# Kernel tuning notes

Hardware: AMD Instinct MI355X
Metric: run time of the kernel (lower is better)

The kernel has to match this reference:

```python
import jax, jax.numpy as jnp
import numpy as np

N, DIN, DOUT = 8192, 512, 256


def setup_inputs() -> dict:
    key = jax.random.key(0)
    ks = jax.random.split(key, 8)
    s_in = 1.0 / np.sqrt(DIN)   # ~ torch Linear default init scale
    s_out = 1.0 / np.sqrt(DOUT)
    return {
        "x": jax.random.normal(ks[0], (N, DIN), jnp.float32),
        "Wm": jax.random.normal(ks[1], (DIN, DOUT), jnp.float32) * s_in,
        "Wn": jax.random.normal(ks[2], (DIN, DOUT), jnp.float32) * s_in,
        "Wr": jax.random.normal(ks[3], (DIN, DOUT), jnp.float32) * s_in,
        "Wt": jax.random.normal(ks[4], (DIN, DOUT), jnp.float32) * s_in,
        "Wrg": jax.random.normal(ks[5], (DOUT, DOUT), jnp.float32) * s_out,
        "brg": jnp.zeros((DOUT,), jnp.float32),
        "Wlg": jax.random.normal(ks[6], (DOUT, DOUT), jnp.float32) * s_out,
        "blg": jnp.zeros((DOUT,), jnp.float32),
        "Wp": jax.random.normal(ks[7], (DOUT, 1), jnp.float32) * s_out,
        "bp": jnp.zeros((1,), jnp.float32),
    }


def reference(x, Wm, Wn, Wr, Wt, Wrg, brg, Wlg, blg, Wp, bp):
    n = x.shape[0]
    xm = x @ Wm                      # [N, 256]
    xn = x @ Wn                      # [N, 256]
    # pairwise Euclidean distance via GEMM trick (avoids O(N^2*D) diff tensor)
    sq = (jnp.sum(xm * xm, axis=-1)[:, None]
          + jnp.sum(xn * xn, axis=-1)[None, :]
          - 2.0 * (xm @ xn.T))       # [N, N]
    dist = jnp.sqrt(jnp.maximum(sq, 0.0)) * 0.5
    exps = jnp.exp(-dist) / (n / 64.0)
    eye = jnp.eye(n, dtype=x.dtype)
    adj = exps * (1.0 - eye) + eye   # unit diagonal, scaled off-diagonal
    xr = adj @ (x @ Wr)              # graph conv: [N,N]@[N,256]
    xl = x @ Wt
    w = jax.nn.sigmoid(xr @ Wrg + brg + xl @ Wlg + blg)
    feat = (1.0 - w) * xr + w * xl   # gated fusion
    score = feat @ Wp + bp           # [N, 1]
    return adj, score
```

## Files before the change

### kernel.cpp

```cpp
#include <hip/hip_runtime.h>
#include <stdint.h>

typedef __attribute__((ext_vector_type(8))) short bf16x8;
typedef __attribute__((ext_vector_type(4))) float f32x4;

__device__ __forceinline__ unsigned short f2bf(float f){
  unsigned u = __float_as_uint(f);
  u += 0x7FFFu + ((u >> 16) & 1u);
  return (unsigned short)(u >> 16);
}
__device__ __forceinline__ float bf2f(unsigned short s){
  return __uint_as_float(((unsigned)s) << 16);
}

__device__ __forceinline__ int lds_off(int r, int b){
  return r * 128 + (b ^ ((r & 7) << 4));
}

__device__ __forceinline__ void cp16(const unsigned short* g, unsigned short* l){
  __builtin_amdgcn_global_load_lds(
      (const __attribute__((address_space(1))) unsigned int*)g,
      (__attribute__((address_space(3))) unsigned int*)l, 16, 0, 0);
}

template<int ROWS, int NT>
__device__ __forceinline__ void stage_async(unsigned short* lds, const unsigned short* g,
                                            long row0, long stride, long k0, int tid){
#pragma unroll
  for (int c = tid; c < ROWS * 8; c += NT){
    int r = c >> 3, s = c & 7;
    int ss = s ^ (r & 7);
    cp16(g + (row0 + r) * stride + k0 + ss * 8, lds + (long)(c & ~63) * 8);
  }
}

template<int ROWS, int NT>
__device__ __forceinline__ void stage_f32_nt(unsigned short* lds, const float* g,
                                             long row0, long stride, long k0, int tid){
#pragma unroll
  for (int c = tid; c < ROWS * 8; c += NT){
    int r = c >> 3, s = c & 7;
    const f32x4* src = (const f32x4*)(g + (row0 + r) * stride + k0 + s * 8);
    f32x4 v0 = __builtin_nontemporal_load(src);
    f32x4 v1 = __builtin_nontemporal_load(src + 1);
    unsigned short t[8] = { f2bf(v0[0]), f2bf(v0[1]), f2bf(v0[2]), f2bf(v0[3]),
                            f2bf(v1[0]), f2bf(v1[1]), f2bf(v1[2]), f2bf(v1[3]) };
    *(uint4*)((char*)lds + lds_off(r, s * 16)) = *(const uint4*)t;
  }
}

__device__ __forceinline__ int xcd_swz(int bid, int nwg){
  int q = nwg >> 3;
  return (bid & 7) * q + (bid >> 3);
}

__global__ __launch_bounds__(256) void k_prep(const float* x, const float* Wm, const float* Wn,
    const float* Wr, const float* Wt, const float* Wrg, const float* Wlg, const float* bp,
    unsigned short* WT, unsigned short* WcatT, unsigned short* xbf, float* score){
  long id = (long)blockIdx.x * 256 + threadIdx.x;
  if (id < 1024L * 512){
    int n = (int)(id >> 9), k = (int)(id & 511);
    const float* W = (n < 256) ? Wm : ((n < 512) ? Wn : ((n < 768) ? Wr : Wt));
    WT[id] = f2bf(W[(long)k * 256 + (n & 255)]);
  }
  if (id < 256L * 512){
    int n = (int)(id >> 9), k = (int)(id & 511);
    WcatT[id] = f2bf(k < 256 ? Wrg[(long)k * 256 + n] : Wlg[(long)(k - 256) * 256 + n]);
  }
  if (id < 8192) score[id] = bp[0];
  long xe = id * 8;
  float4 v0 = *(const float4*)(x + xe);
  float4 v1 = *(const float4*)(x + xe + 4);
  unsigned short t[8] = { f2bf(v0.x), f2bf(v0.y), f2bf(v0.z), f2bf(v0.w),
                          f2bf(v1.x), f2bf(v1.y), f2bf(v1.z), f2bf(v1.w) };
  *(uint4*)(xbf + xe) = *(const uint4*)t;
}

__global__ __launch_bounds__(256, 3) void k_gemmA(const unsigned short* xbf, const unsigned short* WT,
    unsigned short* xm, unsigned short* xn, unsigned short* xwrT, unsigned short* xl){
  __shared__ unsigned short ldsA[128 * 64];
  __shared__ unsigned short ldsB[128 * 64];
  int tid = threadIdx.x, lane = tid & 63, w = tid >> 6;
  int r = lane & 15, gq = lane >> 4;
  int wi = w >> 1, wc = w & 1;
  int swz = xcd_swz(blockIdx.x, 512);
  int bm = swz & 63, bn = swz >> 6;

  f32x4 acc[4][4];
  f32x4 zero = {0.f, 0.f, 0.f, 0.f};
#pragma unroll
  for (int m = 0; m < 4; ++m)
#pragma unroll
    for (int n = 0; n < 4; ++n) acc[m][n] = zero;

  for (int k0 = 0; k0 < 512; k0 += 64){
    __syncthreads();
    stage_async<128, 256>(ldsA, xbf, (long)bm * 128, 512, k0, tid);
    stage_async<128, 256>(ldsB, WT, (long)bn * 128, 512, k0, tid);
    __syncthreads();
#pragma unroll
    for (int ks = 0; ks < 2; ++ks){
      int bb = ks * 64 + gq * 16;
      bf16x8 a[4], b[4];
#pragma unroll
      for (int m = 0; m < 4; ++m)
        a[m] = *(const bf16x8*)((const char*)ldsA + lds_off(wi * 64 + m * 16 + r, bb));
#pragma unroll
      for (int n = 0; n < 4; ++n)
        b[n] = *(const bf16x8*)((const char*)ldsB + lds_off(wc * 64 + n * 16 + r, bb));
#pragma unroll
      for (int m = 0; m < 4; ++m)
#pragma unroll
        for (int n = 0; n < 4; ++n)
          acc[m][n] = __builtin_amdgcn_mfma_f32_16x16x32_bf16(b[n], a[m], acc[m][n], 0, 0, 0);
    }
  }
#pragma unroll
  for (int m = 0; m < 4; ++m){
    int i = bm * 128 + wi * 64 + m * 16 + r;
#pragma unroll
    for (int n = 0; n < 4; ++n){
      int ng = bn * 128 + wc * 64 + n * 16 + gq * 4;
      int sector = ng >> 8, nc = ng & 255;
      unsigned short p[4] = { f2bf(acc[m][n][0]), f2bf(acc[m][n][1]),
                              f2bf(acc[m][n][2]), f2bf(acc[m][n][3]) };
      if (sector == 2){
#pragma unroll
        for (int q = 0; q < 4; ++q) xwrT[(long)(nc + q) * 8192 + i] = p[q];
      } else {
        unsigned short* dst = sector == 0 ? xm : (sector == 1 ? xn : xl);
        *(uint2*)(dst + (long)i * 256 + nc) = *(const uint2*)p;
      }
    }
  }
}

__global__ __launch_bounds__(256) void k_norms(const unsigned short* xm, const unsigned short* xn,
                                               float* nm, float* nn){
  int w = threadIdx.x >> 6, lane = threadIdx.x & 63;
  int row = blockIdx.x * 4 + w;
  const unsigned short* src = (row < 8192) ? xm : xn;
  int rr = row & 8191;
  unsigned short v[4];
  *(uint2*)v = *(const uint2*)(src + (long)rr * 256 + lane * 4);
  float s = 0.f;
#pragma unroll
  for (int t = 0; t < 4; ++t){ float f = bf2f(v[t]); s += f * f; }
#pragma unroll
  for (int o = 32; o; o >>= 1) s += __shfl_xor(s, o);
  if (lane == 0) ((row < 8192) ? nm : nn)[rr] = s;
}

__global__ __launch_bounds__(256, 4) void k_adj(const unsigned short* xm, const unsigned short* xn,
    const float* nm, const float* nn, float* adj){
  __shared__ char smem[32768];
  unsigned short* ldsA = (unsigned short*)smem;
  unsigned short* ldsB = (unsigned short*)(smem + 16384);
  f32x4* ldsOut = (f32x4*)smem;

  int tid = threadIdx.x, lane = tid & 63, w = tid >> 6;
  int r = lane & 15, gq = lane >> 4;
  int wi = w >> 1, wj = w & 1;
  int swz = xcd_swz(blockIdx.x, 4096);
  int bm = swz & 63, bn = swz >> 6;

  f32x4 acc1[4][4];
  f32x4 zero = {0.f, 0.f, 0.f, 0.f};
#pragma unroll
  for (int m = 0; m < 4; ++m)
#pragma unroll
    for (int n = 0; n < 4; ++n) acc1[m][n] = zero;

  for (int k0 = 0; k0 < 256; k0 += 64){
    __syncthreads();
    stage_async<128, 256>(ldsA, xm, (long)bm * 128, 256, k0, tid);
    stage_async<128, 256>(ldsB, xn, (long)bn * 128, 256, k0, tid);
    __syncthreads();
#pragma unroll
    for (int ks = 0; ks < 2; ++ks){
      int bb = ks * 64 + gq * 16;
      bf16x8 a[4], b[4];
#pragma unroll
      for (int m = 0; m < 4; ++m)
        a[m] = *(const bf16x8*)((const char*)ldsA + lds_off(wi * 64 + m * 16 + r, bb));
#pragma unroll
      for (int n = 0; n < 4; ++n)
        b[n] = *(const bf16x8*)((const char*)ldsB + lds_off(wj * 64 + n * 16 + r, bb));
#pragma unroll
      for (int m = 0; m < 4; ++m)
#pragma unroll
        for (int n = 0; n < 4; ++n)
          acc1[m][n] = __builtin_amdgcn_mfma_f32_16x16x32_bf16(b[n], a[m], acc1[m][n], 0, 0, 0);
    }
  }

  float nmi[4];
#pragma unroll
  for (int m = 0; m < 4; ++m) nmi[m] = nm[bm * 128 + wi * 64 + m * 16 + r];
#pragma unroll
  for (int n = 0; n < 4; ++n){
    int jb = bn * 128 + wj * 64 + n * 16 + gq * 4;
    float4 nn4 = *(const float4*)(nn + jb);
    const float nnq[4] = { nn4.x, nn4.y, nn4.z, nn4.w };
#pragma unroll
    for (int m = 0; m < 4; ++m){
      int i = bm * 128 + wi * 64 + m * 16 + r;
#pragma unroll
      for (int q = 0; q < 4; ++q){
        float sq = nmi[m] + nnq[q] - 2.f * acc1[m][n][q];
        float d = sqrtf(fmaxf(sq, 0.f)) * 0.5f;
        acc1[m][n][q] = (i == jb + q) ? 1.f : __expf(-d) * (1.f / 128.f);
      }
    }
  }

#pragma unroll
  for (int p = 0; p < 2; ++p){
    __syncthreads();
    if (wi == p){
#pragma unroll
      for (int m = 0; m < 4; ++m){
        int row64 = m * 16 + r;
#pragma unroll
        for (int n = 0; n < 4; ++n){
          int slot = wj * 16 + n * 4 + gq;
          ldsOut[row64 * 32 + (slot ^ (row64 & 7))] = acc1[m][n];
        }
      }
    }
    __syncthreads();
#pragma unroll
    for (int c = 0; c < 8; ++c){
      int rr = w * 16 + ((lane >> 3) << 1) + (c & 1);
      int slot = (c >> 1) * 8 + (lane & 7);
      f32x4 v = ldsOut[rr * 32 + (slot ^ (rr & 7))];
      long grow = (long)(bm * 128 + p * 64 + rr) * 8192 + bn * 128 + slot * 4;
      __builtin_nontemporal_store(v, (f32x4*)(adj + grow));
    }
  }
}

__global__ __launch_bounds__(512, 2) void k_xr(const float* adj,
    const unsigned short* xwrT, float* partial, int klen, int nblk){
  __shared__ unsigned short ldsA[128 * 64];
  __shared__ unsigned short ldsB[256 * 64];
  int tid = threadIdx.x, lane = tid & 63, w = tid >> 6;
  int r = lane & 15, gq = lane >> 4;
  int wi = w >> 2, wc = w & 3;
  int swz = xcd_swz(blockIdx.x, nblk);
  int bm = swz & 63, sp = swz >> 6;
  long j0 = (long)sp * klen;

  f32x4 acc[4][4];
  f32x4 zero = {0.f, 0.f, 0.f, 0.f};
#pragma unroll
  for (int m = 0; m < 4; ++m)
#pragma unroll
    for (int n = 0; n < 4; ++n) acc[m][n] = zero;

  for (int k0 = 0; k0 < klen; k0 += 64){
    __syncthreads();
    stage_f32_nt<128, 512>(ldsA, adj, (long)bm * 128, 8192, j0 + k0, tid);
    stage_async<256, 512>(ldsB, xwrT, 0, 8192, j0 + k0, tid);
    __syncthreads();
#pragma unroll
    for (int ks = 0; ks < 2; ++ks){
      int bb = ks * 64 + gq * 16;
      bf16x8 a[4], b[4];
#pragma unroll
      for (int m = 0; m < 4; ++m)
        a[m] = *(const bf16x8*)((const char*)ldsA + lds_off(wi * 64 + m * 16 + r, bb));
#pragma unroll
      for (int n = 0; n < 4; ++n)
        b[n] = *(const bf16x8*)((const char*)ldsB + lds_off(wc * 64 + n * 16 + r, bb));
#pragma unroll
      for (int m = 0; m < 4; ++m)
#pragma unroll
        for (int n = 0; n < 4; ++n)
          acc[m][n] = __builtin_amdgcn_mfma_f32_16x16x32_bf16(b[n], a[m], acc[m][n], 0, 0, 0);
    }
  }
  float* dst = partial + (long)sp * 8192 * 256;
#pragma unroll
  for (int m = 0; m < 4; ++m){
    int i = bm * 128 + wi * 64 + m * 16 + r;
#pragma unroll
    for (int n = 0; n < 4; ++n){
      int cb = wc * 64 + n * 16 + gq * 4;
      __builtin_nontemporal_store(acc[m][n], (f32x4*)(dst + (long)i * 256 + cb));
    }
  }
}

__global__ __launch_bounds__(256) void k_reduce_xr(const float* partial, unsigned short* xr, int S){
  long idx = ((long)blockIdx.x * 256 + threadIdx.x) * 4;
  f32x4 a = __builtin_nontemporal_load((const f32x4*)(partial + idx));
  for (int s = 1; s < S; ++s){
    f32x4 b = __builtin_nontemporal_load((const f32x4*)(partial + (long)s * 8192 * 256 + idx));
    a += b;
  }
  unsigned short p[4] = { f2bf(a[0]), f2bf(a[1]), f2bf(a[2]), f2bf(a[3]) };
  *(uint2*)(xr + idx) = make_uint2((unsigned)p[0] | ((unsigned)p[1] << 16),
                                   (unsigned)p[2] | ((unsigned)p[3] << 16));
}

__global__ __launch_bounds__(512, 2) void k_gate(const unsigned short* xr, const unsigned short* xl,
    const unsigned short* WcatT, const float* brg, const float* blg,
    const float* Wp, float* score){
  __shared__ unsigned short ldsA[128 * 64];
  __shared__ unsigned short ldsB[256 * 64];
  int tid = threadIdx.x, lane = tid & 63, w = tid >> 6;
  int r = lane & 15, gq = lane >> 4;
  int wi = w >> 2, wc = w & 3;
  int bm = blockIdx.x;

  f32x4 acc[4][4];
  f32x4 zero = {0.f, 0.f, 0.f, 0.f};
#pragma unroll
  for (int m = 0; m < 4; ++m)
#pragma unroll
    for (int n = 0; n < 4; ++n) acc[m][n] = zero;

  for (int k0 = 0; k0 < 512; k0 += 64){
    const unsigned short* A = (k0 < 256) ? xr : xl;
    __syncthreads();
    stage_async<128, 512>(ldsA, A, (long)bm * 128, 256, k0 & 255, tid);
    stage_async<256, 512>(ldsB, WcatT, 0, 512, k0, tid);
    __syncthreads();
#pragma unroll
    for (int ks = 0; ks < 2; ++ks){
      int bb = ks * 64 + gq * 16;
      bf16x8 a[4], b[4];
#pragma unroll
      for (int m = 0; m < 4; ++m)
        a[m] = *(const bf16x8*)((const char*)ldsA + lds_off(wi * 64 + m * 16 + r, bb));
#pragma unroll
      for (int n = 0; n < 4; ++n)
        b[n] = *(const bf16x8*)((const char*)ldsB + lds_off(wc * 64 + n * 16 + r, bb));
#pragma unroll
      for (int m = 0; m < 4; ++m)
#pragma unroll
        for (int n = 0; n < 4; ++n)
          acc[m][n] = __builtin_amdgcn_mfma_f32_16x16x32_bf16(b[n], a[m], acc[m][n], 0, 0, 0);
    }
  }
#pragma unroll
  for (int m = 0; m < 4; ++m){
    int i = bm * 128 + wi * 64 + m * 16 + r;
    float part = 0.f;
#pragma unroll
    for (int n = 0; n < 4; ++n){
      int cb = wc * 64 + n * 16 + gq * 4;
      float4 b4  = *(const float4*)(brg + cb);
      float4 l4  = *(const float4*)(blg + cb);
      float4 wp4 = *(const float4*)(Wp + cb);
      unsigned short xr4[4], xl4[4];
      *(uint2*)xr4 = *(const uint2*)(xr + (long)i * 256 + cb);
      *(uint2*)xl4 = *(const uint2*)(xl + (long)i * 256 + cb);
      const float bq[4] = { b4.x, b4.y, b4.z, b4.w };
      const float lq[4] = { l4.x, l4.y, l4.z, l4.w };
      const float pq[4] = { wp4.x, wp4.y, wp4.z, wp4.w };
#pragma unroll
      for (int q = 0; q < 4; ++q){
        float arg = acc[m][n][q] + bq[q] + lq[q];
        float wv = 1.f / (1.f + __expf(-arg));
        float feat = (1.f - wv) * bf2f(xr4[q]) + wv * bf2f(xl4[q]);
        part += feat * pq[q];
      }
    }
    part += __shfl_xor(part, 16);
    part += __shfl_xor(part, 32);
    if (gq == 0) atomicAdd(score + i, part);
  }
}

extern "C" void kernel_launch(void* const* d_in, const int* in_sizes, int n_in,
                              void* d_out, int out_size, void* d_ws, size_t ws_size,
                              hipStream_t stream){
  const float* x   = (const float*)d_in[0];
  const float* Wm  = (const float*)d_in[1];
  const float* Wn  = (const float*)d_in[2];
  const float* Wr  = (const float*)d_in[3];
  const float* Wt  = (const float*)d_in[4];
  const float* Wrg = (const float*)d_in[5];
  const float* brg = (const float*)d_in[6];
  const float* Wlg = (const float*)d_in[7];
  const float* blg = (const float*)d_in[8];
  const float* Wp  = (const float*)d_in[9];
  const float* bp  = (const float*)d_in[10];

  float* adj   = (float*)d_out;
  float* score = adj + 8192L * 8192;

  char* wsb = (char*)d_ws;
  unsigned short* xm    = (unsigned short*)(wsb);
  unsigned short* xn    = (unsigned short*)(wsb + (4L  << 20));
  unsigned short* xwrT  = (unsigned short*)(wsb + (8L  << 20));
  unsigned short* xl    = (unsigned short*)(wsb + (12L << 20));
  unsigned short* xr    = (unsigned short*)(wsb + (16L << 20));
  float*          nm    = (float*)         (wsb + (20L << 20));
  float*          nn    = nm + 8192;
  unsigned short* WT    = (unsigned short*)(wsb + (21L << 20));
  unsigned short* WcatT = (unsigned short*)(wsb + (22L << 20));
  unsigned short* xbf   = (unsigned short*)(wsb + (23L << 20));
  float*          partial = (float*)(wsb + (31L << 20));

  int NS = 1;
  size_t base = 31L << 20;
  if      (ws_size >= base + 8 * (8L << 20)) NS = 8;
  else if (ws_size >= base + 4 * (8L << 20)) NS = 4;
  else if (ws_size >= base + 2 * (8L << 20)) NS = 2;

  k_prep  <<<2048, 256, 0, stream>>>(x, Wm, Wn, Wr, Wt, Wrg, Wlg, bp, WT, WcatT, xbf, score);
  k_gemmA <<<512, 256, 0, stream>>>(xbf, WT, xm, xn, xwrT, xl);
  k_norms <<<4096, 256, 0, stream>>>(xm, xn, nm, nn);
  k_adj   <<<4096, 256, 0, stream>>>(xm, xn, nm, nn, adj);
  k_xr    <<<64 * NS, 512, 0, stream>>>(adj, xwrT, partial, 8192 / NS, 64 * NS);
  k_reduce_xr<<<2048, 256, 0, stream>>>(partial, xr, NS);
  k_gate  <<<64, 512, 0, stream>>>(xr, xl, WcatT, brg, blg, Wp, score);
}
```

Measured before the change: 307.3 us.

## Fuse adjacency computation with graph-conv GEMM, keeping adj tile in LDS

Merges the adjacency kernel and the adj@xWr GEMM into one kernel. Each block loops over column tiles of its row band, computes the exp-distance tile, stores it to LDS as bf16 and writes it to global memory. It then uses that LDS tile directly as the A operand of the second GEMM, so the full fp32 adj matrix is no longer read back from HBM. The costs are fewer, longer-running blocks (64*NSP), serialized per-block work, and an adj output that is now rounded to bf16 before being widened to fp32. It also adds s_setprio around the MFMA loops.

```diff
diff --git a/kernel.cpp b/kernel.cpp
--- a/kernel.cpp
+++ b/kernel.cpp
@@ -16,6 +16,9 @@
 __device__ __forceinline__ int lds_off(int r, int b){
   return r * 128 + (b ^ ((r & 7) << 4));
 }
+__device__ __forceinline__ int ldsP_off(int r, int b){
+  return r * 256 + (b ^ ((r & 7) << 4));
+}
 
 __device__ __forceinline__ void cp16(const unsigned short* g, unsigned short* l){
   __builtin_amdgcn_global_load_lds(
@@ -31,21 +34,6 @@
     int r = c >> 3, s = c & 7;
     int ss = s ^ (r & 7);
     cp16(g + (row0 + r) * stride + k0 + ss * 8, lds + (long)(c & ~63) * 8);
-  }
-}
-
-template<int ROWS, int NT>
-__device__ __forceinline__ void stage_f32_nt(unsigned short* lds, const float* g,
-                                             long row0, long stride, long k0, int tid){
-#pragma unroll
-  for (int c = tid; c < ROWS * 8; c += NT){
-    int r = c >> 3, s = c & 7;
-    const f32x4* src = (const f32x4*)(g + (row0 + r) * stride + k0 + s * 8);
-    f32x4 v0 = __builtin_nontemporal_load(src);
-    f32x4 v1 = __builtin_nontemporal_load(src + 1);
-    unsigned short t[8] = { f2bf(v0[0]), f2bf(v0[1]), f2bf(v0[2]), f2bf(v0[3]),
-                            f2bf(v1[0]), f2bf(v1[1]), f2bf(v1[2]), f2bf(v1[3]) };
-    *(uint4*)((char*)lds + lds_off(r, s * 16)) = *(const uint4*)t;
   }
 }
 
@@ -151,143 +139,133 @@
   if (lane == 0) ((row < 8192) ? nm : nn)[rr] = s;
 }
 
-__global__ __launch_bounds__(256, 4) void k_adj(const unsigned short* xm, const unsigned short* xn,
-    const float* nm, const float* nn, float* adj){
-  __shared__ char smem[32768];
+__global__ __launch_bounds__(256, 2) void k_fused(
+    const unsigned short* xm, const unsigned short* xn,
+    const float* nm, const float* nn, const unsigned short* xwrT,
+    float* adj, float* partial, int ntiles, int nsp){
+  __shared__ char smem[65536];
   unsigned short* ldsA = (unsigned short*)smem;
   unsigned short* ldsB = (unsigned short*)(smem + 16384);
-  f32x4* ldsOut = (f32x4*)smem;
+  unsigned short* ldsW = (unsigned short*)smem;
+  char*           ldsP = smem + 32768;
 
   int tid = threadIdx.x, lane = tid & 63, w = tid >> 6;
   int r = lane & 15, gq = lane >> 4;
   int wi = w >> 1, wj = w & 1;
-  int swz = xcd_swz(blockIdx.x, 4096);
-  int bm = swz & 63, bn = swz >> 6;
-
-  f32x4 acc1[4][4];
+  int sp = blockIdx.x % nsp, bm = blockIdx.x / nsp;
+
   f32x4 zero = {0.f, 0.f, 0.f, 0.f};
+  f32x4 acc2[4][8];
 #pragma unroll
   for (int m = 0; m < 4; ++m)
 #pragma unroll
-    for (int n = 0; n < 4; ++n) acc1[m][n] = zero;
-
-  for (int k0 = 0; k0 < 256; k0 += 64){
-    __syncthreads();
-    stage_async<128, 256>(ldsA, xm, (long)bm * 128, 256, k0, tid);
-    stage_async<128, 256>(ldsB, xn, (long)bn * 128, 256, k0, tid);
-    __syncthreads();
-#pragma unroll
-    for (int ks = 0; ks < 2; ++ks){
-      int bb = ks * 64 + gq * 16;
-      bf16x8 a[4], b[4];
-#pragma unroll
-      for (int m = 0; m < 4; ++m)
-        a[m] = *(const bf16x8*)((const char*)ldsA + lds_off(wi * 64 + m * 16 + r, bb));
-#pragma unroll
-      for (int n = 0; n < 4; ++n)
-        b[n] = *(const bf16x8*)((const char*)ldsB + lds_off(wj * 64 + n * 16 + r, bb));
-#pragma unroll
-      for (int m = 0; m < 4; ++m)
+    for (int n = 0; n < 8; ++n) acc2[m][n] = zero;
+
+  float nmi[4];
+#pragma unroll
+  for (int m = 0; m < 4; ++m) nmi[m] = nm[bm * 128 + wi * 64 + m * 16 + r];
+
+  for (int t = 0; t < ntiles; ++t){
+    int bn = sp * ntiles + t;
+    f32x4 acc1[4][4];
+#pragma unroll
+    for (int m = 0; m < 4; ++m)
+#pragma unroll
+      for (int n = 0; n < 4; ++n) acc1[m][n] = zero;
+
+    for (int k0 = 0; k0 < 256; k0 += 64){
+      __syncthreads();
+      stage_async<128, 256>(ldsA, xm, (long)bm * 128, 256, k0, tid);
+      stage_async<128, 256>(ldsB, xn, (long)bn * 128, 256, k0, tid);
+      __syncthreads();
+      __builtin_amdgcn_s_setprio(1);
+#pragma unroll
+      for (int ks = 0; ks < 2; ++ks){
+        int bb = ks * 64 + gq * 16;
+        bf16x8 a[4], b[4];
+#pragma unroll
+        for (int m = 0; m < 4; ++m)
+          a[m] = *(const bf16x8*)((const char*)ldsA + lds_off(wi * 64 + m * 16 + r, bb));
 #pragma unroll
         for (int n = 0; n < 4; ++n)
-          acc1[m][n] = __builtin_amdgcn_mfma_f32_16x16x32_bf16(b[n], a[m], acc1[m][n], 0, 0, 0);
-    }
-  }
-
-  float nmi[4];
-#pragma unroll
-  for (int m = 0; m < 4; ++m) nmi[m] = nm[bm * 128 + wi * 64 + m * 16 + r];
-#pragma unroll
-  for (int n = 0; n < 4; ++n){
-    int jb = bn * 128 + wj * 64 + n * 16 + gq * 4;
-    float4 nn4 = *(const float4*)(nn + jb);
-    const float nnq[4] = { nn4.x, nn4.y, nn4.z, nn4.w };
-#pragma unroll
-    for (int m = 0; m < 4; ++m){
-      int i = bm * 128 + wi * 64 + m * 16 + r;
-#pragma unroll
-      for (int q = 0; q < 4; ++q){
-        float sq = nmi[m] + nnq[q] - 2.f * acc1[m][n][q];
-        float d = sqrtf(fmaxf(sq, 0.f)) * 0.5f;
-        acc1[m][n][q] = (i == jb + q) ? 1.f : __expf(-d) * (1.f / 128.f);
-      }
-    }
-  }
-
-#pragma unroll
-  for (int p = 0; p < 2; ++p){
-    __syncthreads();
-    if (wi == p){
+          b[n] = *(const bf16x8*)((const char*)ldsB + lds_off(wj * 64 + n * 16 + r, bb));
+#pragma unroll
+        for (int m = 0; m < 4; ++m)
+#pragma unroll
+          for (int n = 0; n < 4; ++n)
+            acc1[m][n] = __builtin_amdgcn_mfma_f32_16x16x32_bf16(b[n], a[m], acc1[m][n], 0, 0, 0);
+      }
+      __builtin_amdgcn_s_setprio(0);
+    }
+
+#pragma unroll
+    for (int n = 0; n < 4; ++n){
+      int jl0 = wj * 64 + n * 16 + gq * 4;
+      int jb = bn * 128 + jl0;
+      float4 nn4 = *(const float4*)(nn + jb);
+      const float nnq[4] = { nn4.x, nn4.y, nn4.z, nn4.w };
 #pragma unroll
       for (int m = 0; m < 4; ++m){
-        int row64 = m * 16 + r;
-#pragma unroll
-        for (int n = 0; n < 4; ++n){
-          int slot = wj * 16 + n * 4 + gq;
-          ldsOut[row64 * 32 + (slot ^ (row64 & 7))] = acc1[m][n];
+        int il = wi * 64 + m * 16 + r;
+        int i = bm * 128 + il;
+        unsigned short pv[4];
+#pragma unroll
+        for (int q = 0; q < 4; ++q){
+          float sq = nmi[m] + nnq[q] - 2.f * acc1[m][n][q];
+          float d = sqrtf(fmaxf(sq, 0.f)) * 0.5f;
+          float v = (i == jb + q) ? 1.f : __expf(-d) * (1.f / 128.f);
+          pv[q] = f2bf(v);
         }
-      }
-    }
-    __syncthreads();
-#pragma unroll
-    for (int c = 0; c < 8; ++c){
-      int rr = w * 16 + ((lane >> 3) << 1) + (c & 1);
-      int slot = (c >> 1) * 8 + (lane & 7);
-      f32x4 v = ldsOut[rr * 32 + (slot ^ (rr & 7))];
-      long grow = (long)(bm * 128 + p * 64 + rr) * 8192 + bn * 128 + slot * 4;
+        *(uint2*)(ldsP + ldsP_off(il, jl0 * 2)) = *(const uint2*)pv;
+      }
+    }
+    __syncthreads();
+
+#pragma unroll
+    for (int o = 0; o < 16; ++o){
+      int seg = o * 256 + tid;
+      int row = seg >> 5, js = seg & 31;
+      unsigned short pb[4];
+      *(uint2*)pb = *(const uint2*)(ldsP + ldsP_off(row, js * 8));
+      f32x4 v = { bf2f(pb[0]), bf2f(pb[1]), bf2f(pb[2]), bf2f(pb[3]) };
+      long grow = (long)(bm * 128 + row) * 8192 + (long)bn * 128 + js * 4;
       __builtin_nontemporal_store(v, (f32x4*)(adj + grow));
     }
-  }
-}
-
-__global__ __launch_bounds__(512, 2) void k_xr(const float* adj,
-    const unsigned short* xwrT, float* partial, int klen, int nblk){
-  __shared__ unsigned short ldsA[128 * 64];
-  __shared__ unsigned short ldsB[256 * 64];
-  int tid = threadIdx.x, lane = tid & 63, w = tid >> 6;
-  int r = lane & 15, gq = lane >> 4;
-  int wi = w >> 2, wc = w & 3;
-  int swz = xcd_swz(blockIdx.x, nblk);
-  int bm = swz & 63, sp = swz >> 6;
-  long j0 = (long)sp * klen;
-
-  f32x4 acc[4][4];
-  f32x4 zero = {0.f, 0.f, 0.f, 0.f};
-#pragma unroll
-  for (int m = 0; m < 4; ++m)
-#pragma unroll
-    for (int n = 0; n < 4; ++n) acc[m][n] = zero;
-
-  for (int k0 = 0; k0 < klen; k0 += 64){
-    __syncthreads();
-    stage_f32_nt<128, 512>(ldsA, adj, (long)bm * 128, 8192, j0 + k0, tid);
-    stage_async<256, 512>(ldsB, xwrT, 0, 8192, j0 + k0, tid);
-    __syncthreads();
-#pragma unroll
-    for (int ks = 0; ks < 2; ++ks){
-      int bb = ks * 64 + gq * 16;
-      bf16x8 a[4], b[4];
-#pragma unroll
-      for (int m = 0; m < 4; ++m)
-        a[m] = *(const bf16x8*)((const char*)ldsA + lds_off(wi * 64 + m * 16 + r, bb));
-#pragma unroll
-      for (int n = 0; n < 4; ++n)
-        b[n] = *(const bf16x8*)((const char*)ldsB + lds_off(wc * 64 + n * 16 + r, bb));
-#pragma unroll
-      for (int m = 0; m < 4; ++m)
-#pragma unroll
-        for (int n = 0; n < 4; ++n)
-          acc[m][n] = __builtin_amdgcn_mfma_f32_16x16x32_bf16(b[n], a[m], acc[m][n], 0, 0, 0);
-    }
-  }
+
+    int wm2 = w >> 1, wn2 = w & 1;
+    for (int kh = 0; kh < 2; ++kh){
+      __syncthreads();
+      stage_async<256, 256>(ldsW, xwrT, 0, 8192, (long)bn * 128 + kh * 64, tid);
+      __syncthreads();
+      __builtin_amdgcn_s_setprio(1);
+#pragma unroll
+      for (int ks = 0; ks < 2; ++ks){
+        bf16x8 a[4], b[8];
+#pragma unroll
+        for (int m = 0; m < 4; ++m)
+          a[m] = *(const bf16x8*)(ldsP + ldsP_off(wm2 * 64 + m * 16 + r, kh * 128 + ks * 64 + gq * 16));
+#pragma unroll
+        for (int n = 0; n < 8; ++n)
+          b[n] = *(const bf16x8*)((const char*)ldsW + lds_off(wn2 * 128 + n * 16 + r, ks * 64 + gq * 16));
+#pragma unroll
+        for (int m = 0; m < 4; ++m)
+#pragma unroll
+          for (int n = 0; n < 8; ++n)
+            acc2[m][n] = __builtin_amdgcn_mfma_f32_16x16x32_bf16(b[n], a[m], acc2[m][n], 0, 0, 0);
+      }
+      __builtin_amdgcn_s_setprio(0);
+    }
+  }
+
+  int wm2 = w >> 1, wn2 = w & 1;
   float* dst = partial + (long)sp * 8192 * 256;
 #pragma unroll
   for (int m = 0; m < 4; ++m){
-    int i = bm * 128 + wi * 64 + m * 16 + r;
-#pragma unroll
-    for (int n = 0; n < 4; ++n){
-      int cb = wc * 64 + n * 16 + gq * 4;
-      __builtin_nontemporal_store(acc[m][n], (f32x4*)(dst + (long)i * 256 + cb));
+    int i = bm * 128 + wm2 * 64 + m * 16 + r;
+#pragma unroll
+    for (int n = 0; n < 8; ++n){
+      int c = wn2 * 128 + n * 16 + gq * 4;
+      __builtin_nontemporal_store(acc2[m][n], (f32x4*)(dst + (long)i * 256 + c));
     }
   }
 }
@@ -405,17 +383,16 @@
   unsigned short* xbf   = (unsigned short*)(wsb + (23L << 20));
   float*          partial = (float*)(wsb + (31L << 20));
 
-  int NS = 1;
+  int NSP = 1;
   size_t base = 31L << 20;
-  if      (ws_size >= base + 8 * (8L << 20)) NS = 8;
-  else if (ws_size >= base + 4 * (8L << 20)) NS = 4;
-  else if (ws_size >= base + 2 * (8L << 20)) NS = 2;
+  if      (ws_size >= base + 8 * (8L << 20)) NSP = 8;
+  else if (ws_size >= base + 4 * (8L << 20)) NSP = 4;
+  else if (ws_size >= base + 2 * (8L << 20)) NSP = 2;
 
   k_prep  <<<2048, 256, 0, stream>>>(x, Wm, Wn, Wr, Wt, Wrg, Wlg, bp, WT, WcatT, xbf, score);
   k_gemmA <<<512, 256, 0, stream>>>(xbf, WT, xm, xn, xwrT, xl);
   k_norms <<<4096, 256, 0, stream>>>(xm, xn, nm, nn);
-  k_adj   <<<4096, 256, 0, stream>>>(xm, xn, nm, nn, adj);
-  k_xr    <<<64 * NS, 512, 0, stream>>>(adj, xwrT, partial, 8192 / NS, 64 * NS);
-  k_reduce_xr<<<2048, 256, 0, stream>>>(partial, xr, NS);
+  k_fused <<<64 * NSP, 256, 0, stream>>>(xm, xn, nm, nn, xwrT, adj, partial, 64 / NSP, NSP);
+  k_reduce_xr<<<2048, 256, 0, stream>>>(partial, xr, NSP);
   k_gate  <<<64, 512, 0, stream>>>(xr, xl, WcatT, brg, blg, Wp, score);
 }
```

Result: slower. 451.5 us (+46.9%).

## Double-buffer k_adj and k_xr staging and fuse row norms into gemmA

Applied to the files above, without the earlier changes.

k_adj and k_xr now use double-buffered LDS: the next K tile is prefetched while MFMAs run on the current one, and wave priority is raised during the math. In k_xr the fp32 adj loads go into registers and are converted to bf16 after the MFMAs, which hides the global latency. Row norms are computed in the gemmA epilogue with atomics, so the separate k_norms kernel is gone, and the split-K count is capped at 4. The larger LDS use lowers occupancy (k_adj drops to 2 blocks, k_xr to 1). Norms are now taken from fp32 accumulators rather than the bf16-rounded values, and atomic summation order can vary between runs.

```diff
diff --git a/kernel.cpp b/kernel.cpp
--- a/kernel.cpp
+++ b/kernel.cpp
@@ -34,18 +34,19 @@
   }
 }
 
-template<int ROWS, int NT>
-__device__ __forceinline__ void stage_f32_nt(unsigned short* lds, const float* g,
-                                             long row0, long stride, long k0, int tid){
-#pragma unroll
-  for (int c = tid; c < ROWS * 8; c += NT){
-    int r = c >> 3, s = c & 7;
-    const f32x4* src = (const f32x4*)(g + (row0 + r) * stride + k0 + s * 8);
+template<int NT>
+__device__ __forceinline__ void stage_adj(unsigned short* lds, const float* adj,
+                                          long row0, long j, int tid){
+#pragma unroll
+  for (int u = 0; u < 1024 / NT; ++u){
+    int c = tid + u * NT;
+    int rr = c >> 3, s = c & 7;
+    const f32x4* src = (const f32x4*)(adj + (row0 + rr) * 8192 + j + s * 8);
     f32x4 v0 = __builtin_nontemporal_load(src);
     f32x4 v1 = __builtin_nontemporal_load(src + 1);
-    unsigned short t[8] = { f2bf(v0[0]), f2bf(v0[1]), f2bf(v0[2]), f2bf(v0[3]),
-                            f2bf(v1[0]), f2bf(v1[1]), f2bf(v1[2]), f2bf(v1[3]) };
-    *(uint4*)((char*)lds + lds_off(r, s * 16)) = *(const uint4*)t;
+    unsigned short tb[8] = { f2bf(v0[0]), f2bf(v0[1]), f2bf(v0[2]), f2bf(v0[3]),
+                             f2bf(v1[0]), f2bf(v1[1]), f2bf(v1[2]), f2bf(v1[3]) };
+    *(uint4*)((char*)lds + lds_off(rr, s * 16)) = *(const uint4*)tb;
   }
 }
 
@@ -56,7 +57,8 @@
 
 __global__ __launch_bounds__(256) void k_prep(const float* x, const float* Wm, const float* Wn,
     const float* Wr, const float* Wt, const float* Wrg, const float* Wlg, const float* bp,
-    unsigned short* WT, unsigned short* WcatT, unsigned short* xbf, float* score){
+    unsigned short* WT, unsigned short* WcatT, unsigned short* xbf, float* nm, float* nn,
+    float* score){
   long id = (long)blockIdx.x * 256 + threadIdx.x;
   if (id < 1024L * 512){
     int n = (int)(id >> 9), k = (int)(id & 511);
@@ -67,7 +69,7 @@
     int n = (int)(id >> 9), k = (int)(id & 511);
     WcatT[id] = f2bf(k < 256 ? Wrg[(long)k * 256 + n] : Wlg[(long)(k - 256) * 256 + n]);
   }
-  if (id < 8192) score[id] = bp[0];
+  if (id < 8192){ score[id] = bp[0]; nm[id] = 0.f; nn[id] = 0.f; }
   long xe = id * 8;
   float4 v0 = *(const float4*)(x + xe);
   float4 v1 = *(const float4*)(x + xe + 4);
@@ -77,7 +79,8 @@
 }
 
 __global__ __launch_bounds__(256, 3) void k_gemmA(const unsigned short* xbf, const unsigned short* WT,
-    unsigned short* xm, unsigned short* xn, unsigned short* xwrT, unsigned short* xl){
+    unsigned short* xm, unsigned short* xn, unsigned short* xwrT, unsigned short* xl,
+    float* nm, float* nn){
   __shared__ unsigned short ldsA[128 * 64];
   __shared__ unsigned short ldsB[128 * 64];
   int tid = threadIdx.x, lane = tid & 63, w = tid >> 6;
@@ -132,30 +135,22 @@
         *(uint2*)(dst + (long)i * 256 + nc) = *(const uint2*)p;
       }
     }
-  }
-}
-
-__global__ __launch_bounds__(256) void k_norms(const unsigned short* xm, const unsigned short* xn,
-                                               float* nm, float* nn){
-  int w = threadIdx.x >> 6, lane = threadIdx.x & 63;
-  int row = blockIdx.x * 4 + w;
-  const unsigned short* src = (row < 8192) ? xm : xn;
-  int rr = row & 8191;
-  unsigned short v[4];
-  *(uint2*)v = *(const uint2*)(src + (long)rr * 256 + lane * 4);
-  float s = 0.f;
-#pragma unroll
-  for (int t = 0; t < 4; ++t){ float f = bf2f(v[t]); s += f * f; }
-#pragma unroll
-  for (int o = 32; o; o >>= 1) s += __shfl_xor(s, o);
-  if (lane == 0) ((row < 8192) ? nm : nn)[rr] = s;
-}
-
-__global__ __launch_bounds__(256, 4) void k_adj(const unsigned short* xm, const unsigned short* xn,
+    if (bn < 4){
+      float s = 0.f;
+#pragma unroll
+      for (int n = 0; n < 4; ++n)
+#pragma unroll
+        for (int q = 0; q < 4; ++q) s += acc[m][n][q] * acc[m][n][q];
+      s += __shfl_xor(s, 16);
+      s += __shfl_xor(s, 32);
+      if (gq == 0) atomicAdd(((bn < 2) ? nm : nn) + i, s);
+    }
+  }
+}
+
+__global__ __launch_bounds__(256, 2) void k_adj(const unsigned short* xm, const unsigned short* xn,
     const float* nm, const float* nn, float* adj){
-  __shared__ char smem[32768];
-  unsigned short* ldsA = (unsigned short*)smem;
-  unsigned short* ldsB = (unsigned short*)(smem + 16384);
+  __shared__ char smem[65536];
   f32x4* ldsOut = (f32x4*)smem;
 
   int tid = threadIdx.x, lane = tid & 63, w = tid >> 6;
@@ -171,11 +166,21 @@
 #pragma unroll
     for (int n = 0; n < 4; ++n) acc1[m][n] = zero;
 
-  for (int k0 = 0; k0 < 256; k0 += 64){
-    __syncthreads();
-    stage_async<128, 256>(ldsA, xm, (long)bm * 128, 256, k0, tid);
-    stage_async<128, 256>(ldsB, xn, (long)bn * 128, 256, k0, tid);
-    __syncthreads();
+  stage_async<128, 256>((unsigned short*)smem, xm, (long)bm * 128, 256, 0, tid);
+  stage_async<128, 256>((unsigned short*)(smem + 16384), xn, (long)bn * 128, 256, 0, tid);
+  __syncthreads();
+
+#pragma unroll
+  for (int t = 0; t < 4; ++t){
+    char* cbuf = smem + (t & 1) * 32768;
+    if (t < 3){
+      char* nbuf = smem + ((t + 1) & 1) * 32768;
+      stage_async<128, 256>((unsigned short*)nbuf, xm, (long)bm * 128, 256, (t + 1) * 64, tid);
+      stage_async<128, 256>((unsigned short*)(nbuf + 16384), xn, (long)bn * 128, 256, (t + 1) * 64, tid);
+    }
+    unsigned short* ldsA = (unsigned short*)cbuf;
+    unsigned short* ldsB = (unsigned short*)(cbuf + 16384);
+    __builtin_amdgcn_s_setprio(1);
 #pragma unroll
     for (int ks = 0; ks < 2; ++ks){
       int bb = ks * 64 + gq * 16;
@@ -192,6 +197,8 @@
         for (int n = 0; n < 4; ++n)
           acc1[m][n] = __builtin_amdgcn_mfma_f32_16x16x32_bf16(b[n], a[m], acc1[m][n], 0, 0, 0);
     }
+    __builtin_amdgcn_s_setprio(0);
+    __syncthreads();
   }
 
   float nmi[4];
@@ -240,16 +247,16 @@
   }
 }
 
-__global__ __launch_bounds__(512, 2) void k_xr(const float* adj,
+__global__ __launch_bounds__(512, 1) void k_xr(const float* adj,
     const unsigned short* xwrT, float* partial, int klen, int nblk){
-  __shared__ unsigned short ldsA[128 * 64];
-  __shared__ unsigned short ldsB[256 * 64];
+  __shared__ char smem[98304];
   int tid = threadIdx.x, lane = tid & 63, w = tid >> 6;
   int r = lane & 15, gq = lane >> 4;
   int wi = w >> 2, wc = w & 3;
   int swz = xcd_swz(blockIdx.x, nblk);
   int bm = swz & 63, sp = swz >> 6;
   long j0 = (long)sp * klen;
+  int nt = klen >> 6;
 
   f32x4 acc[4][4];
   f32x4 zero = {0.f, 0.f, 0.f, 0.f};
@@ -258,11 +265,31 @@
 #pragma unroll
     for (int n = 0; n < 4; ++n) acc[m][n] = zero;
 
-  for (int k0 = 0; k0 < klen; k0 += 64){
-    __syncthreads();
-    stage_f32_nt<128, 512>(ldsA, adj, (long)bm * 128, 8192, j0 + k0, tid);
-    stage_async<256, 512>(ldsB, xwrT, 0, 8192, j0 + k0, tid);
-    __syncthreads();
+  stage_adj<512>((unsigned short*)smem, adj, (long)bm * 128, j0, tid);
+  stage_async<256, 512>((unsigned short*)(smem + 16384), xwrT, 0, 8192, j0, tid);
+  __syncthreads();
+
+  for (int t = 0; t < nt; ++t){
+    char* cbuf = smem + (t & 1) * 49152;
+    char* nbuf = smem + ((t & 1) ^ 1) * 49152;
+    bool pf = (t + 1 < nt);
+    long jn = j0 + (long)(t + 1) * 64;
+    f32x4 av0[2], av1[2];
+    int rra[2], ssa[2];
+    if (pf){
+#pragma unroll
+      for (int u = 0; u < 2; ++u){
+        int c = tid + u * 512;
+        rra[u] = c >> 3; ssa[u] = c & 7;
+        const f32x4* src = (const f32x4*)(adj + (long)(bm * 128 + rra[u]) * 8192 + jn + ssa[u] * 8);
+        av0[u] = __builtin_nontemporal_load(src);
+        av1[u] = __builtin_nontemporal_load(src + 1);
+      }
+      stage_async<256, 512>((unsigned short*)(nbuf + 16384), xwrT, 0, 8192, jn, tid);
+    }
+    unsigned short* ldsA = (unsigned short*)cbuf;
+    unsigned short* ldsB = (unsigned short*)(cbuf + 16384);
+    __builtin_amdgcn_s_setprio(1);
 #pragma unroll
     for (int ks = 0; ks < 2; ++ks){
       int bb = ks * 64 + gq * 16;
@@ -279,7 +306,18 @@
         for (int n = 0; n < 4; ++n)
           acc[m][n] = __builtin_amdgcn_mfma_f32_16x16x32_bf16(b[n], a[m], acc[m][n], 0, 0, 0);
     }
-  }
+    __builtin_amdgcn_s_setprio(0);
+    if (pf){
+#pragma unroll
+      for (int u = 0; u < 2; ++u){
+        unsigned short tb[8] = { f2bf(av0[u][0]), f2bf(av0[u][1]), f2bf(av0[u][2]), f2bf(av0[u][3]),
+                                 f2bf(av1[u][0]), f2bf(av1[u][1]), f2bf(av1[u][2]), f2bf(av1[u][3]) };
+        *(uint4*)(nbuf + lds_off(rra[u], ssa[u] * 16)) = *(const uint4*)tb;
+      }
+    }
+    __syncthreads();
+  }
+
   float* dst = partial + (long)sp * 8192 * 256;
 #pragma unroll
   for (int m = 0; m < 4; ++m){
@@ -407,13 +445,11 @@
 
   int NS = 1;
   size_t base = 31L << 20;
-  if      (ws_size >= base + 8 * (8L << 20)) NS = 8;
-  else if (ws_size >= base + 4 * (8L << 20)) NS = 4;
+  if      (ws_size >= base + 4 * (8L << 20)) NS = 4;
   else if (ws_size >= base + 2 * (8L << 20)) NS = 2;
 
-  k_prep  <<<2048, 256, 0, stream>>>(x, Wm, Wn, Wr, Wt, Wrg, Wlg, bp, WT, WcatT, xbf, score);
-  k_gemmA <<<512, 256, 0, stream>>>(xbf, WT, xm, xn, xwrT, xl);
-  k_norms <<<4096, 256, 0, stream>>>(xm, xn, nm, nn);
+  k_prep  <<<2048, 256, 0, stream>>>(x, Wm, Wn, Wr, Wt, Wrg, Wlg, bp, WT, WcatT, xbf, nm, nn, score);
+  k_gemmA <<<512, 256, 0, stream>>>(xbf, WT, xm, xn, xwrT, xl, nm, nn);
   k_adj   <<<4096, 256, 0, stream>>>(xm, xn, nm, nn, adj);
   k_xr    <<<64 * NS, 512, 0, stream>>>(adj, xwrT, partial, 8192 / NS, 64 * NS);
   k_reduce_xr<<<2048, 256, 0, stream>>>(partial, xr, NS);
```

Result: faster. 261.6 us, median of 2 (-14.9%).
